# Optimization experiments

Hardware: AMD Instinct MI355X
Metric: run time of the kernel (lower is better)

The kernel has to match this reference:

```python
import jax, jax.numpy as jnp
import numpy as np

DIM = 512
NE = 16
SEQ = 4096


def _linear_params(key, fan_in, fan_out):
    kw, kb = jax.random.split(key)
    scale = 1.0 / np.sqrt(fan_in)
    W = jax.random.uniform(kw, (fan_out, fan_in), jnp.float32, -scale, scale)
    b = jax.random.uniform(kb, (fan_out,), jnp.float32, -scale, scale)
    return W, b


def setup_inputs() -> dict:
    key = jax.random.key(0)
    ks = jax.random.split(key, 9)
    h = jax.random.normal(ks[0], (1, 1, 3 * DIM), jnp.float32)
    us = jax.random.normal(ks[1], (1, 1, DIM), jnp.float32)
    ue = jax.random.normal(ks[2], (1, 1, DIM), jnp.float32)
    u = jax.random.normal(ks[3], (1, SEQ, 2 * DIM), jnp.float32)
    noise = jax.random.normal(ks[4], (1, SEQ, DIM, NE), jnp.float32)
    W_nn, b_nn = _linear_params(ks[5], 3 * DIM, NE * DIM)
    W_no, b_no = _linear_params(ks[6], 3 * DIM, NE * DIM)
    W_E, b_E = _linear_params(ks[7], 3 * DIM, NE * DIM)
    W_r, b_r = _linear_params(ks[8], 5 * DIM, DIM)
    return {"h": h, "us": us, "ue": ue, "u": u, "noise": noise,
            "W_nn": W_nn, "b_nn": b_nn, "W_no": W_no, "b_no": b_no,
            "W_E": W_E, "b_E": b_E, "W_r": W_r, "b_r": b_r}


def _sparsify(m):
    # m: [1, S, dim, NE]; top-2 over experts, keep those entries, softmax with
    # large negative fill on zeros (faithful to torch code incl. the ==0 test).
    _, idx = jax.lax.top_k(m, 2)                       # [1,S,dim,2]
    one_hot = jax.nn.one_hot(idx, NE, dtype=m.dtype).sum(-2)  # [1,S,dim,NE]
    out = m * one_hot
    out = out + (-100000.0) * (out == 0).astype(m.dtype)
    return jax.nn.softmax(out, axis=-1)


def reference(h, us, ue, u, noise, W_nn, b_nn, W_no, b_no, W_E, b_E, W_r, b_r):
    S = u.shape[1]
    R = jnp.concatenate((h, us, ue), axis=-1) @ W_r.T + b_r   # [1,1,dim]
    R = jnp.broadcast_to(R, (R.shape[0], S, R.shape[2]))      # [1,S,dim]
    x = jnp.concatenate((u, R), axis=-1)                      # [1,S,3*dim]
    h1 = (x @ W_nn.T + b_nn).reshape(1, -1, DIM, NE)
    h2 = (x @ W_no.T + b_no).reshape(1, -1, DIM, NE) * noise
    g = _sparsify(h1 + h2)
    e = (x @ W_E.T + b_E).reshape(1, S, DIM, NE)
    return (g * e).mean(-1)                                   # [1,S,dim]
```

## Files before the change

kernel.cpp:

```cpp
#include <hip/hip_runtime.h>
#include <hip/hip_bf16.h>
#include <math.h>

#define DIMD 512
#define SEQL 4096
#define KU 1024
#define KF 1536
#define NJ 8192
#define KC 384
#define NTK 32

#define BM 64
#define BK 32
#define PA 33
#define PW 68

#define GAP_T 1e-4f

#define WS_R    0u
#define WS_BC   4096u
#define WS_BCE  69632u
#define WS_CNT  102400u
#define WS_WL   102656u
#define WS_UHI  8491264u
#define WS_ULO  16879872u
#define WS_WHI  25268480u
#define WS_WLO  58822912u
#define WS_WEH  92377344u
#define WS_NEEDED 109154560u

typedef __attribute__((ext_vector_type(8))) short bf16x8;
typedef __attribute__((ext_vector_type(4))) float f32x4;

__device__ __forceinline__ ushort f2bf(float f) {
    __hip_bfloat16 h = __float2bfloat16(f);
    return *reinterpret_cast<ushort*>(&h);
}
__device__ __forceinline__ float bf2f(ushort v) {
    unsigned int b = ((unsigned int)v) << 16;
    return __uint_as_float(b);
}

__device__ __forceinline__ float chainR(
    const float* __restrict__ h, const float* __restrict__ us, const float* __restrict__ ue,
    const float* __restrict__ Wr, const float* __restrict__ br, int o)
{
    float accT = 0.f;
    for (int k0 = 0; k0 < 2560; k0 += KC) {
        int ke = (k0 + KC < 2560) ? k0 + KC : 2560;
        float accC = 0.f;
        for (int k = k0; k < ke; ++k) {
            float xv = (k < 1536) ? h[k] : (k < 2048) ? us[k - 1536] : ue[k - 2048];
            accC = fmaf(xv, Wr[(size_t)o * 2560 + k], accC);
        }
        accT = __fadd_rn(accT, accC);
    }
    return __fadd_rn(accT, br[o]);
}

#define KCP 385
__global__ __launch_bounds__(256) void k_R32(
    const float* __restrict__ h, const float* __restrict__ us, const float* __restrict__ ue,
    const float* __restrict__ Wr, const float* __restrict__ br,
    float* __restrict__ Rout, int* __restrict__ cnt)
{
    __shared__ float xs[2560];
    __shared__ float Wsh[64 * KCP];
    if (blockIdx.x == 0 && threadIdx.x == 0) *cnt = 0;
    const int tid = threadIdx.x;
    const int o0 = blockIdx.x * 64;
    for (int k = tid; k < 2560; k += 256)
        xs[k] = (k < 1536) ? h[k] : (k < 2048) ? us[k - 1536] : ue[k - 2048];
    float accT = 0.f;
    for (int c = 0; c < 7; ++c) {
        int k0 = c * KC;
        int len = (k0 + KC <= 2560) ? KC : (2560 - k0);
        __syncthreads();
        for (int idx = tid * 4; idx < 64 * len; idx += 1024) {
            int r = idx / len, kk = idx - r * len;
            *(float4*)&Wsh[r * KCP + kk] = *(const float4*)&Wr[(size_t)(o0 + r) * 2560 + k0 + kk];
        }
        __syncthreads();
        if (tid < 64) {
            float accC = 0.f;
            for (int k = 0; k < len; ++k)
                accC = fmaf(xs[k0 + k], Wsh[tid * KCP + k], accC);
            accT = __fadd_rn(accT, accC);
        }
    }
    if (tid < 64) Rout[o0 + tid] = __fadd_rn(accT, br[o0 + tid]);
}

#define LPAD 1032
__global__ __launch_bounds__(256) void k_prep_u(
    const float* __restrict__ u, ushort* __restrict__ uhi, ushort* __restrict__ ulo)
{
    __shared__ ushort hs[16 * LPAD], ls[16 * LPAD];
    const int tid = threadIdx.x;
    const int t16 = blockIdx.x;
    #pragma unroll
    for (int it = 0; it < 16; ++it) {
        int k = tid * 4;
        float4 v = *(const float4*)&u[((size_t)t16 * 16 + it) * KU + k];
        ushort4 a, b;
        a.x = f2bf(v.x); b.x = f2bf(v.x - bf2f(a.x));
        a.y = f2bf(v.y); b.y = f2bf(v.y - bf2f(a.y));
        a.z = f2bf(v.z); b.z = f2bf(v.z - bf2f(a.z));
        a.w = f2bf(v.w); b.w = f2bf(v.w - bf2f(a.w));
        *(ushort4*)&hs[it * LPAD + k] = a;
        *(ushort4*)&ls[it * LPAD + k] = b;
    }
    __syncthreads();
    #pragma unroll
    for (int ct = 0; ct < 8; ++ct) {
        int c = ct * 256 + tid;
        int k32 = c >> 6, l = c & 63;
        int src = (l & 15) * LPAD + k32 * 32 + (l >> 4) * 8;
        size_t dst = (((size_t)t16 * NTK + k32) * 64 + l) * 8;
        *(uint4*)&uhi[dst] = *(const uint4*)&hs[src];
        *(uint4*)&ulo[dst] = *(const uint4*)&ls[src];
    }
}

__global__ __launch_bounds__(256) void k_prep_w(
    const float* __restrict__ Wnn, const float* __restrict__ Wno,
    ushort* __restrict__ whi, ushort* __restrict__ wlo)
{
    __shared__ ushort hs[16 * LPAD], ls[16 * LPAD];
    const int tid = threadIdx.x;
    const int mat = blockIdx.x >> 9, j16 = blockIdx.x & 511;
    const float* W = mat ? Wno : Wnn;
    #pragma unroll
    for (int it = 0; it < 16; ++it) {
        int k = tid * 4;
        float4 v = *(const float4*)&W[((size_t)j16 * 16 + it) * KF + k];
        ushort4 a, b;
        a.x = f2bf(v.x); b.x = f2bf(v.x - bf2f(a.x));
        a.y = f2bf(v.y); b.y = f2bf(v.y - bf2f(a.y));
        a.z = f2bf(v.z); b.z = f2bf(v.z - bf2f(a.z));
        a.w = f2bf(v.w); b.w = f2bf(v.w - bf2f(a.w));
        *(ushort4*)&hs[it * LPAD + k] = a;
        *(ushort4*)&ls[it * LPAD + k] = b;
    }
    __syncthreads();
    #pragma unroll
    for (int ct = 0; ct < 8; ++ct) {
        int c = ct * 256 + tid;
        int k32 = c >> 6, l = c & 63;
        int src = (l & 15) * LPAD + k32 * 32 + (l >> 4) * 8;
        size_t dst = ((((size_t)mat * 512 + j16) * NTK + k32) * 64 + l) * 8;
        *(uint4*)&whi[dst] = *(const uint4*)&hs[src];
        *(uint4*)&wlo[dst] = *(const uint4*)&ls[src];
    }
}

__global__ __launch_bounds__(256) void k_prep_we(
    const float* __restrict__ WE, ushort* __restrict__ weh)
{
    __shared__ ushort hs[16 * LPAD];
    const int tid = threadIdx.x;
    const int j16 = blockIdx.x;
    #pragma unroll
    for (int it = 0; it < 16; ++it) {
        int k = tid * 4;
        float4 v = *(const float4*)&WE[((size_t)j16 * 16 + it) * KF + k];
        ushort4 a;
        a.x = f2bf(v.x); a.y = f2bf(v.y); a.z = f2bf(v.z); a.w = f2bf(v.w);
        *(ushort4*)&hs[it * LPAD + k] = a;
    }
    __syncthreads();
    #pragma unroll
    for (int ct = 0; ct < 8; ++ct) {
        int c = ct * 256 + tid;
        int k32 = c >> 6, l = c & 63;
        int src = (l & 15) * LPAD + k32 * 32 + (l >> 4) * 8;
        size_t dst = (((size_t)j16 * NTK + k32) * 64 + l) * 8;
        *(uint4*)&weh[dst] = *(const uint4*)&hs[src];
    }
}

__global__ __launch_bounds__(256) void k_bias(
    const float* __restrict__ R32,
    const float* __restrict__ Wnn, const float* __restrict__ Wno, const float* __restrict__ WE,
    const float* __restrict__ bnn, const float* __restrict__ bno, const float* __restrict__ bE,
    float* __restrict__ Bc, float* __restrict__ Bce)
{
    int wid = blockIdx.x * 4 + (threadIdx.x >> 6);
    int l = threadIdx.x & 63;
    int mat = wid >> 13, j = wid & 8191;
    const float* W = (mat == 0) ? Wnn : (mat == 1) ? Wno : WE;
    const float* b = (mat == 0) ? bnn : (mat == 1) ? bno : bE;
    double acc = 0.0;
    for (int k = 1024 + l; k < 1536; k += 64)
        acc += (double)R32[k - KU] * (double)W[(size_t)j * KF + k];
    for (int off = 32; off > 0; off >>= 1) acc += __shfl_down(acc, off);
    if (l == 0) {
        float r = (float)(acc + (double)b[j]);
        if (mat < 2) Bc[wid] = r; else Bce[j] = r;
    }
}

struct MSt {
    ushort u1[4096], u2[4096];
    ushort w1[4096], w2[4096];
    ushort we[2048];
};

__global__ __launch_bounds__(256, 3) void k_m(
    const ushort* __restrict__ uhi, const ushort* __restrict__ ulo,
    const ushort* __restrict__ whi, const ushort* __restrict__ wlo,
    const ushort* __restrict__ weh,
    const float* __restrict__ noise,
    const float* __restrict__ Bc, const float* __restrict__ Bce,
    int* __restrict__ cnt, int* __restrict__ wl, float* __restrict__ out)
{
    __shared__ MSt sm;
    const int tid = threadIdx.x;
    const int w = tid >> 6, l = tid & 63;
    const int wm = w >> 1, wn = w & 1;
    const int lr = l & 15, lq = l >> 4;
    const int l8 = l * 8;
    const int sBase = blockIdx.y * 128;
    const int sB16 = blockIdx.y * 8;
    const int jBase = blockIdx.x * 64;
    const int jB16 = blockIdx.x * 4;
    const int dBase = jBase >> 4;

    f32x4 acc1[4][2] = {}, acc2[4][2] = {}, accE[4][2] = {};

    for (int kt = 0; kt < NTK; ++kt) {
        __syncthreads();
        #pragma unroll
        for (int it = 0; it < 4; ++it) {
            int c = tid + it * 256;
            int buf = c >> 9, rem = c & 511;
            size_t g = (((size_t)(sB16 + (rem >> 6)) * NTK + kt) * 64 + (rem & 63)) * 8;
            const ushort* src = buf ? ulo : uhi;
            ushort* dst = (buf ? sm.u2 : sm.u1) + rem * 8;
            *(uint4*)dst = *(const uint4*)&src[g];
        }
        #pragma unroll
        for (int it = 0; it < 4; ++it) {
            int c = tid + it * 256;
            int buf = c >> 9, rem = c & 511;
            int mt = rem >> 8, jt = (rem >> 6) & 3;
            size_t g = ((((size_t)mt * 512 + jB16 + jt) * NTK + kt) * 64 + (rem & 63)) * 8;
            const ushort* src = buf ? wlo : whi;
            ushort* dst = (buf ? sm.w2 : sm.w1) + rem * 8;
            *(uint4*)dst = *(const uint4*)&src[g];
        }
        {
            int jt = tid >> 6;
            size_t g = (((size_t)(jB16 + jt) * NTK + kt) * 64 + (tid & 63)) * 8;
            *(uint4*)&sm.we[tid * 8] = *(const uint4*)&weh[g];
        }
        __syncthreads();
        bf16x8 a1[4], a2[4];
        #pragma unroll
        for (int i = 0; i < 4; ++i) {
            int base = (wm * 4 + i) * 512 + l8;
            a1[i] = *(const bf16x8*)&sm.u1[base];
            a2[i] = *(const bf16x8*)&sm.u2[base];
        }
        #pragma unroll
        for (int n = 0; n < 2; ++n) {
            int jloc = wn * 2 + n;
            {
                bf16x8 p1 = *(const bf16x8*)&sm.w1[jloc * 512 + l8];
                bf16x8 p2 = *(const bf16x8*)&sm.w2[jloc * 512 + l8];
                #pragma unroll
                for (int i = 0; i < 4; ++i) {
                    acc1[i][n] = __builtin_amdgcn_mfma_f32_16x16x32_bf16(a1[i], p1, acc1[i][n], 0, 0, 0);
                    acc1[i][n] = __builtin_amdgcn_mfma_f32_16x16x32_bf16(a1[i], p2, acc1[i][n], 0, 0, 0);
                    acc1[i][n] = __builtin_amdgcn_mfma_f32_16x16x32_bf16(a2[i], p1, acc1[i][n], 0, 0, 0);
                }
            }
            {
                bf16x8 p1 = *(const bf16x8*)&sm.w1[(4 + jloc) * 512 + l8];
                bf16x8 p2 = *(const bf16x8*)&sm.w2[(4 + jloc) * 512 + l8];
                #pragma unroll
                for (int i = 0; i < 4; ++i) {
                    acc2[i][n] = __builtin_amdgcn_mfma_f32_16x16x32_bf16(a1[i], p1, acc2[i][n], 0, 0, 0);
                    acc2[i][n] = __builtin_amdgcn_mfma_f32_16x16x32_bf16(a1[i], p2, acc2[i][n], 0, 0, 0);
                    acc2[i][n] = __builtin_amdgcn_mfma_f32_16x16x32_bf16(a2[i], p1, acc2[i][n], 0, 0, 0);
                }
            }
            {
                bf16x8 pe = *(const bf16x8*)&sm.we[jloc * 512 + l8];
                #pragma unroll
                for (int i = 0; i < 4; ++i)
                    accE[i][n] = __builtin_amdgcn_mfma_f32_16x16x32_bf16(a1[i], pe, accE[i][n], 0, 0, 0);
            }
        }
    }

    float bc1[2], bc2[2], be[2];
    #pragma unroll
    for (int n = 0; n < 2; ++n) {
        int col = jBase + wn * 32 + n * 16 + lr;
        bc1[n] = Bc[col];
        bc2[n] = Bc[NJ + col];
        be[n]  = Bce[col];
    }
    const int gbase = l & 48;
    #pragma unroll
    for (int i = 0; i < 4; ++i)
        #pragma unroll
        for (int n = 0; n < 2; ++n) {
            int colL = wn * 32 + n * 16 + lr;
            int dloc = wn * 2 + n;
            #pragma unroll
            for (int r = 0; r < 4; ++r) {
                int rowL = wm * 64 + i * 16 + lq * 4 + r;
                float m1 = acc1[i][n][r] + bc1[n];
                float m2 = acc2[i][n][r] + bc2[n];
                float nz = noise[(size_t)(sBase + rowL) * NJ + jBase + colL];
                float m  = fmaf(m2, nz, m1);
                float ev = accE[i][n][r] + be[n];
                float v1 = m; int i1 = lr;
                #pragma unroll
                for (int mk = 1; mk <= 8; mk <<= 1) {
                    float ov = __shfl_xor(v1, mk);
                    int oi = __shfl_xor(i1, mk);
                    if (ov > v1 || (ov == v1 && oi < i1)) { v1 = ov; i1 = oi; }
                }
                float v2 = (lr == i1) ? -INFINITY : m;
                int i2 = (lr == i1) ? 64 : lr;
                #pragma unroll
                for (int mk = 1; mk <= 8; mk <<= 1) {
                    float ov = __shfl_xor(v2, mk);
                    int oi = __shfl_xor(i2, mk);
                    if (ov > v2 || (ov == v2 && oi < i2)) { v2 = ov; i2 = oi; }
                }
                float v3 = (lr == i1 || lr == i2) ? -INFINITY : m;
                #pragma unroll
                for (int mk = 1; mk <= 8; mk <<= 1)
                    v3 = fmaxf(v3, __shfl_xor(v3, mk));
                float ev1 = __shfl(ev, gbase + i1);
                float ev2 = __shfl(ev, gbase + (i2 & 15));
                if (lr == 0) {
                    int gidx = (sBase + rowL) * DIMD + dBase + dloc;
                    bool flg = (v2 - v3 < GAP_T) || (fabsf(v1) < GAP_T) || (fabsf(v2) < GAP_T);
                    if (flg) {
                        int pos = atomicAdd(cnt, 1);
                        wl[pos] = gidx;
                    }
                    double x1 = (double)v1, x2 = (double)v2;
                    double vmax = fmax(x1, x2);
                    double g1 = exp(x1 - vmax), g2 = exp(x2 - vmax);
                    double num = g1 * (double)ev1 + g2 * (double)ev2;
                    out[gidx] = (float)(num / (g1 + g2) * 0.0625);
                }
            }
        }
}

__global__ __launch_bounds__(256) void k_repair(
    const float* __restrict__ u, const float* __restrict__ noise,
    const float* __restrict__ Wnn, const float* __restrict__ Wno, const float* __restrict__ WE,
    const float* __restrict__ bnn, const float* __restrict__ bno, const float* __restrict__ bE,
    const float* __restrict__ R32,
    const int* __restrict__ cnt, const int* __restrict__ wl, float* __restrict__ out)
{
    const int l = threadIdx.x & 63;
    const int e = l & 15, mt = l >> 4;
    const int wid = (blockIdx.x * 256 + threadIdx.x) >> 6;
    const int NW = (1024 * 256) >> 6;
    const int n = *cnt;

    for (int i = wid; i < n; i += NW) {
        int si = wl[i];
        int s = si >> 9, d = si & 511;
        int j = d * 16 + e;
        const float* urow = u + (size_t)s * KU;
        float t = 0.f;
        if (mt < 3) {
            const float* Wrow = (mt == 0 ? Wnn : (mt == 1 ? Wno : WE)) + (size_t)j * KF;
            #pragma unroll
            for (int c = 0; c < 4; ++c) {
                float cc = 0.f;
                int k0 = c * KC;
                for (int k = k0; k < k0 + KC; ++k) {
                    float a = (k < KU) ? urow[k] : R32[k - KU];
                    cc = fmaf(a, Wrow[k], cc);
                }
                t = __fadd_rn(t, cc);
            }
            t = __fadd_rn(t, (mt == 0 ? bnn : (mt == 1 ? bno : bE))[j]);
        }
        float h2 = __shfl(t, 16 + e);
        float ee = __shfl(t, 32 + e);
        float m = -INFINITY;
        if (mt == 0)
            m = __fadd_rn(t, __fmul_rn(h2, noise[(size_t)s * NJ + j]));
        float v1 = m; int i1 = e;
        #pragma unroll
        for (int mk = 1; mk <= 8; mk <<= 1) {
            float ov = __shfl_xor(v1, mk);
            int oi = __shfl_xor(i1, mk);
            if (ov > v1 || (ov == v1 && oi < i1)) { v1 = ov; i1 = oi; }
        }
        float v2 = (mt == 0 && e == i1) ? -INFINITY : m;
        int i2 = (mt == 0 && e == i1) ? 64 : e;
        #pragma unroll
        for (int mk = 1; mk <= 8; mk <<= 1) {
            float ov = __shfl_xor(v2, mk);
            int oi = __shfl_xor(i2, mk);
            if (ov > v2 || (ov == v2 && oi < i2)) { v2 = ov; i2 = oi; }
        }
        float se = ee;
        #pragma unroll
        for (int mk = 1; mk <= 8; mk <<= 1) se += __shfl_xor(se, mk);
        float ev1 = __shfl(ee, i1);
        float ev2 = __shfl(ee, i2 & 15);
        if (l == 0) {
            double x1 = (v1 == 0.0f) ? -100000.0 : (double)v1;
            double x2 = (v2 == 0.0f) ? -100000.0 : (double)v2;
            double vmax = fmax(fmax(x1, x2), -100000.0);
            double g1 = exp(x1 - vmax), g2 = exp(x2 - vmax), gz = exp(-100000.0 - vmax);
            double den = g1 + g2 + 14.0 * gz;
            double num = g1 * (double)ev1 + g2 * (double)ev2
                       + gz * ((double)se - (double)ev1 - (double)ev2);
            out[si] = (float)(num / den * 0.0625);
        }
    }
}

__global__ __launch_bounds__(256) void k_base(
    const float* __restrict__ u, const float* __restrict__ noise,
    const float* __restrict__ Wnn, const float* __restrict__ Wno, const float* __restrict__ WE,
    const float* __restrict__ bnn, const float* __restrict__ bno, const float* __restrict__ bE,
    const float* __restrict__ h, const float* __restrict__ us, const float* __restrict__ ue,
    const float* __restrict__ Wr, const float* __restrict__ br,
    float* __restrict__ out)
{
    __shared__ __align__(16) float As[BM][PA];
    __shared__ __align__(16) float Ws[3][BK][PW];
    __shared__ float Rsh[512];

    const int tid = threadIdx.x;
    const int sr = tid >> 2, dl = tid & 3;
    const int jBase = blockIdx.x * 64;
    const int sBase = blockIdx.y * BM;
    const int myCol = dl * 16;

    for (int o = tid; o < 512; o += 256) Rsh[o] = chainR(h, us, ue, Wr, br, o);

    float t1[16] = {}, c1[16] = {}, t2[16] = {}, c2[16] = {}, tE[16] = {}, cE[16] = {};

    for (int kt = 0; kt < KF; kt += BK) {
        __syncthreads();
        if (kt < KU) {
            for (int idx = tid; idx < BM * BK; idx += 256) {
                int r = idx >> 5, c = idx & 31;
                As[r][c] = u[(size_t)(sBase + r) * KU + kt + c];
            }
        }
        for (int idx = tid; idx < 64 * BK; idx += 256) {
            int col = idx >> 5, kk = idx & 31;
            size_t off = (size_t)(jBase + col) * KF + kt + kk;
            Ws[0][kk][col] = Wnn[off];
            Ws[1][kk][col] = Wno[off];
            Ws[2][kk][col] = WE[off];
        }
        __syncthreads();
        const bool uReg = (kt < KU);
        for (int kk = 0; kk < BK; ++kk) {
            float a = uReg ? As[sr][kk] : Rsh[kt + kk - KU];
            #pragma unroll
            for (int q = 0; q < 4; ++q) {
                float4 w0 = *(const float4*)&Ws[0][kk][myCol + 4 * q];
                float4 w1 = *(const float4*)&Ws[1][kk][myCol + 4 * q];
                float4 w2 = *(const float4*)&Ws[2][kk][myCol + 4 * q];
                c1[4*q+0] = fmaf(a, w0.x, c1[4*q+0]);
                c1[4*q+1] = fmaf(a, w0.y, c1[4*q+1]);
                c1[4*q+2] = fmaf(a, w0.z, c1[4*q+2]);
                c1[4*q+3] = fmaf(a, w0.w, c1[4*q+3]);
                c2[4*q+0] = fmaf(a, w1.x, c2[4*q+0]);
                c2[4*q+1] = fmaf(a, w1.y, c2[4*q+1]);
                c2[4*q+2] = fmaf(a, w1.z, c2[4*q+2]);
                c2[4*q+3] = fmaf(a, w1.w, c2[4*q+3]);
                cE[4*q+0] = fmaf(a, w2.x, cE[4*q+0]);
                cE[4*q+1] = fmaf(a, w2.y, cE[4*q+1]);
                cE[4*q+2] = fmaf(a, w2.z, cE[4*q+2]);
                cE[4*q+3] = fmaf(a, w2.w, cE[4*q+3]);
            }
        }
        if (((kt + BK) % KC) == 0 || (kt + BK) == KF) {
            #pragma unroll
            for (int e = 0; e < 16; ++e) {
                t1[e] = __fadd_rn(t1[e], c1[e]); c1[e] = 0.f;
                t2[e] = __fadd_rn(t2[e], c2[e]); c2[e] = 0.f;
                tE[e] = __fadd_rn(tE[e], cE[e]); cE[e] = 0.f;
            }
        }
    }

    const int s = sBase + sr;
    const int jb = jBase + myCol;
    float m32[16]; double evv[16];
    #pragma unroll
    for (int e = 0; e < 16; ++e) {
        float h1 = __fadd_rn(t1[e], bnn[jb + e]);
        float h2 = __fadd_rn(t2[e], bno[jb + e]);
        float nz = noise[(size_t)s * NJ + jb + e];
        m32[e] = __fadd_rn(h1, __fmul_rn(h2, nz));
        evv[e] = (double)__fadd_rn(tE[e], bE[jb + e]);
    }
    int i1 = 0; float v1 = m32[0];
    #pragma unroll
    for (int e = 1; e < 16; ++e) if (m32[e] > v1) { v1 = m32[e]; i1 = e; }
    int i2 = -1; float v2 = -INFINITY;
    #pragma unroll
    for (int e = 0; e < 16; ++e) if (e != i1 && m32[e] > v2) { v2 = m32[e]; i2 = e; }
    double e1 = 0.0, e2 = 0.0, sumE = 0.0;
    #pragma unroll
    for (int e = 0; e < 16; ++e) {
        e1 = (e == i1) ? evv[e] : e1;
        e2 = (e == i2) ? evv[e] : e2;
        sumE += evv[e];
    }
    double x1 = (v1 == 0.0f) ? -100000.0 : (double)v1;
    double x2 = (v2 == 0.0f) ? -100000.0 : (double)v2;
    double vmax = fmax(fmax(x1, x2), -100000.0);
    double g1 = exp(x1 - vmax), g2 = exp(x2 - vmax), gz = exp(-100000.0 - vmax);
    double den = g1 + g2 + 14.0 * gz;
    double num = g1 * e1 + g2 * e2 + gz * (sumE - e1 - e2);
    out[(size_t)s * DIMD + (jBase >> 4) + dl] = (float)(num / den * 0.0625);
}

extern "C" void kernel_launch(void* const* d_in, const int* in_sizes, int n_in,
                              void* d_out, int out_size, void* d_ws, size_t ws_size,
                              hipStream_t stream) {
    (void)in_sizes; (void)n_in; (void)out_size;
    const float* h     = (const float*)d_in[0];
    const float* us    = (const float*)d_in[1];
    const float* ue    = (const float*)d_in[2];
    const float* u     = (const float*)d_in[3];
    const float* noise = (const float*)d_in[4];
    const float* Wnn   = (const float*)d_in[5];
    const float* bnn   = (const float*)d_in[6];
    const float* Wno   = (const float*)d_in[7];
    const float* bno   = (const float*)d_in[8];
    const float* WE    = (const float*)d_in[9];
    const float* bE    = (const float*)d_in[10];
    const float* Wr    = (const float*)d_in[11];
    const float* br    = (const float*)d_in[12];
    float* out = (float*)d_out;

    if (ws_size >= WS_NEEDED) {
        char* ws = (char*)d_ws;
        float* Rws  = (float*)(ws + WS_R);
        float* Bc   = (float*)(ws + WS_BC);
        float* Bce  = (float*)(ws + WS_BCE);
        int*   cnt  = (int*)(ws + WS_CNT);
        int*   wl   = (int*)(ws + WS_WL);
        ushort* uhi = (ushort*)(ws + WS_UHI);
        ushort* ulo = (ushort*)(ws + WS_ULO);
        ushort* whi = (ushort*)(ws + WS_WHI);
        ushort* wlo = (ushort*)(ws + WS_WLO);
        ushort* weh = (ushort*)(ws + WS_WEH);

        hipLaunchKernelGGL(k_R32, dim3(8), dim3(256), 0, stream, h, us, ue, Wr, br, Rws, cnt);
        hipLaunchKernelGGL(k_prep_u, dim3(SEQL / 16), dim3(256), 0, stream, u, uhi, ulo);
        hipLaunchKernelGGL(k_prep_w, dim3(2 * NJ / 16), dim3(256), 0, stream, Wnn, Wno, whi, wlo);
        hipLaunchKernelGGL(k_prep_we, dim3(NJ / 16), dim3(256), 0, stream, WE, weh);
        hipLaunchKernelGGL(k_bias, dim3(6144), dim3(256), 0, stream,
                           Rws, Wnn, Wno, WE, bnn, bno, bE, Bc, Bce);
        hipLaunchKernelGGL(k_m, dim3(NJ / 64, SEQL / 128), dim3(256), 0, stream,
                           uhi, ulo, whi, wlo, weh, noise, Bc, Bce, cnt, wl, out);
        hipLaunchKernelGGL(k_repair, dim3(1024), dim3(256), 0, stream,
                           u, noise, Wnn, Wno, WE, bnn, bno, bE, Rws, cnt, wl, out);
    } else {
        hipLaunchKernelGGL(k_base, dim3(NJ / 64, SEQL / BM), dim3(256), 0, stream,
                           u, noise, Wnn, Wno, WE, bnn, bno, bE,
                           h, us, ue, Wr, br, out);
    }
}
```

Baseline: 808.7 us.

## Prefetch next K-tile into registers while computing current tile

Global loads for the next K tile are issued into nine uint4 registers right after the current tile is stored to shared memory, so their latency can overlap the MFMA work on the current tile. Previously each iteration loaded from global and wrote to LDS serially before computing. This adds 36 VGPRs per thread, which may reduce occupancy.

After: 1.553 ms. +92.1%, slower.

```diff
diff --git a/kernel.cpp b/kernel.cpp
--- a/kernel.cpp
+++ b/kernel.cpp
@@ -228,32 +228,57 @@
 
     f32x4 acc1[4][2] = {}, acc2[4][2] = {}, accE[4][2] = {};
 
+    uint4 rg0, rg1, rg2, rg3, rg4, rg5, rg6, rg7, rg8;
+
+#define LOAD_TILE(kt)                                                                   \
+    {                                                                                   \
+        const size_t kofs = (size_t)(kt) * 512;                                         \
+        {   int c = tid;             int rem = c & 511;                                 \
+            size_t g = (((size_t)(sB16 + (rem >> 6)) * NTK) * 64 + (rem & 63)) * 8;     \
+            rg0 = *(const uint4*)&uhi[g + kofs]; }                                      \
+        {   int c = tid + 256;       int rem = c & 511;                                 \
+            size_t g = (((size_t)(sB16 + (rem >> 6)) * NTK) * 64 + (rem & 63)) * 8;     \
+            rg1 = *(const uint4*)&uhi[g + kofs]; }                                      \
+        {   int c = tid + 512;       int rem = c & 511;                                 \
+            size_t g = (((size_t)(sB16 + (rem >> 6)) * NTK) * 64 + (rem & 63)) * 8;     \
+            rg2 = *(const uint4*)&ulo[g + kofs]; }                                      \
+        {   int c = tid + 768;       int rem = c & 511;                                 \
+            size_t g = (((size_t)(sB16 + (rem >> 6)) * NTK) * 64 + (rem & 63)) * 8;     \
+            rg3 = *(const uint4*)&ulo[g + kofs]; }                                      \
+        {   int rem = tid;           int mt = rem >> 8, jt = (rem >> 6) & 3;            \
+            size_t g = ((((size_t)mt * 512 + jB16 + jt) * NTK) * 64 + (rem & 63)) * 8;  \
+            rg4 = *(const uint4*)&whi[g + kofs]; }                                      \
+        {   int rem = tid + 256;     int mt = rem >> 8, jt = (rem >> 6) & 3;            \
+            size_t g = ((((size_t)mt * 512 + jB16 + jt) * NTK) * 64 + (rem & 63)) * 8;  \
+            rg5 = *(const uint4*)&whi[g + kofs]; }                                      \
+        {   int rem = tid;           int mt = rem >> 8, jt = (rem >> 6) & 3;            \
+            size_t g = ((((size_t)mt * 512 + jB16 + jt) * NTK) * 64 + (rem & 63)) * 8;  \
+            rg6 = *(const uint4*)&wlo[g + kofs]; }                                      \
+        {   int rem = tid + 256;     int mt = rem >> 8, jt = (rem >> 6) & 3;            \
+            size_t g = ((((size_t)mt * 512 + jB16 + jt) * NTK) * 64 + (rem & 63)) * 8;  \
+            rg7 = *(const uint4*)&wlo[g + kofs]; }                                      \
+        {   int jt = tid >> 6;                                                          \
+            size_t g = (((size_t)(jB16 + jt) * NTK) * 64 + (tid & 63)) * 8;             \
+            rg8 = *(const uint4*)&weh[g + kofs]; }                                      \
+    }
+
+    LOAD_TILE(0);
+
     for (int kt = 0; kt < NTK; ++kt) {
         __syncthreads();
-        #pragma unroll
-        for (int it = 0; it < 4; ++it) {
-            int c = tid + it * 256;
-            int buf = c >> 9, rem = c & 511;
-            size_t g = (((size_t)(sB16 + (rem >> 6)) * NTK + kt) * 64 + (rem & 63)) * 8;
-            const ushort* src = buf ? ulo : uhi;
-            ushort* dst = (buf ? sm.u2 : sm.u1) + rem * 8;
-            *(uint4*)dst = *(const uint4*)&src[g];
-        }
-        #pragma unroll
-        for (int it = 0; it < 4; ++it) {
-            int c = tid + it * 256;
-            int buf = c >> 9, rem = c & 511;
-            int mt = rem >> 8, jt = (rem >> 6) & 3;
-            size_t g = ((((size_t)mt * 512 + jB16 + jt) * NTK + kt) * 64 + (rem & 63)) * 8;
-            const ushort* src = buf ? wlo : whi;
-            ushort* dst = (buf ? sm.w2 : sm.w1) + rem * 8;
-            *(uint4*)dst = *(const uint4*)&src[g];
-        }
         {
-            int jt = tid >> 6;
-            size_t g = (((size_t)(jB16 + jt) * NTK + kt) * 64 + (tid & 63)) * 8;
-            *(uint4*)&sm.we[tid * 8] = *(const uint4*)&weh[g];
-        }
+            int rem = tid & 511;
+            *(uint4*)&sm.u1[rem * 8] = rg0;
+            *(uint4*)&sm.u1[(rem + 256) * 8] = rg1;
+            *(uint4*)&sm.u2[rem * 8] = rg2;
+            *(uint4*)&sm.u2[(rem + 256) * 8] = rg3;
+            *(uint4*)&sm.w1[tid * 8] = rg4;
+            *(uint4*)&sm.w1[(tid + 256) * 8] = rg5;
+            *(uint4*)&sm.w2[tid * 8] = rg6;
+            *(uint4*)&sm.w2[(tid + 256) * 8] = rg7;
+            *(uint4*)&sm.we[tid * 8] = rg8;
+        }
+        if (kt + 1 < NTK) LOAD_TILE(kt + 1);
         __syncthreads();
         bf16x8 a1[4], a2[4];
         #pragma unroll
```
